# Performance work log

Hardware: AMD Instinct MI355X
Metric: run time of the kernel (lower is better)

## Reference

```python
import jax, jax.numpy as jnp
import numpy as np

EPS = 1e-5

def _bn(x, w, b, rm, rv):
    # eval-mode BatchNorm over channel axis (x: [..., C] broadcastable)
    return (x - rm) * (w * jax.lax.rsqrt(rv + EPS)) + b

def setup_inputs() -> dict:
    key = jax.random.key(0)
    ks = jax.random.split(key, 20)
    B, C, H, W = 2, 64, 96, 96
    Cq = C // 8  # query/key channels
    Cr = C // 8  # SE reduction channels
    s = 0.05
    inp = {
        'x': jax.random.normal(ks[0], (B, C, H, W), jnp.float32),
        'wq': jax.random.normal(ks[1], (Cq, C), jnp.float32) * s,
        'bq': jnp.zeros((Cq,), jnp.float32),
        'wk': jax.random.normal(ks[2], (Cq, C), jnp.float32) * s,
        'bk': jnp.zeros((Cq,), jnp.float32),
        'wv': jax.random.normal(ks[3], (C, C), jnp.float32) * s,
        'bv': jnp.zeros((C,), jnp.float32),
        'gamma': jnp.full((1,), 0.5, jnp.float32),
        'bn_w': jnp.ones((C,), jnp.float32),
        'bn_b': jnp.zeros((C,), jnp.float32),
        'bn_rm': jax.random.normal(ks[4], (C,), jnp.float32) * 0.1,
        'bn_rv': jax.random.uniform(ks[5], (C,), jnp.float32) + 0.5,
        'se_w1': jax.random.normal(ks[6], (Cr, C), jnp.float32) * s,
        'se_b1': jnp.zeros((Cr,), jnp.float32),
        'se_bn1_w': jnp.ones((Cr,), jnp.float32),
        'se_bn1_b': jnp.zeros((Cr,), jnp.float32),
        'se_bn1_rm': jax.random.normal(ks[7], (Cr,), jnp.float32) * 0.1,
        'se_bn1_rv': jax.random.uniform(ks[8], (Cr,), jnp.float32) + 0.5,
        'se_w2': jax.random.normal(ks[9], (C, Cr), jnp.float32) * s,
        'se_b2': jnp.zeros((C,), jnp.float32),
        'se_bn2_w': jnp.ones((C,), jnp.float32),
        'se_bn2_b': jnp.zeros((C,), jnp.float32),
        'se_bn2_rm': jax.random.normal(ks[10], (C,), jnp.float32) * 0.1,
        'se_bn2_rv': jax.random.uniform(ks[11], (C,), jnp.float32) + 0.5,
    }
    return inp

def reference(x, wq, bq, wk, bk, wv, bv, gamma, bn_w, bn_b, bn_rm, bn_rv,
              se_w1, se_b1, se_bn1_w, se_bn1_b, se_bn1_rm, se_bn1_rv,
              se_w2, se_b2, se_bn2_w, se_bn2_b, se_bn2_rm, se_bn2_rv):
    B, C, H, W = x.shape
    N = H * W
    xf = x.reshape(B, C, N)
    # PAM branch: 1x1 conv projections
    q = jnp.einsum('oc,bcn->bno', wq, xf) + bq            # [B,N,C/8]
    k = jnp.einsum('oc,bcn->bon', wk, xf) + bk[:, None]    # [B,C/8,N]
    v = jnp.einsum('oc,bcn->bon', wv, xf) + bv[:, None]    # [B,C,N]
    energy = jnp.einsum('bno,bom->bnm', q, k)              # [B,N,N]
    attn = jax.nn.softmax(energy, axis=-1)
    # out[b,c,i] = sum_j v[b,c,j] * attn[b,i,j]  (bmm(V, attn^T))
    out = jnp.einsum('bcj,bij->bci', v, attn)
    out = gamma[0] * out
    out = _bn(out, bn_w[:, None], bn_b[:, None], bn_rm[:, None], bn_rv[:, None])
    pam = out.reshape(B, C, H, W)
    # SE branch: GAP + 1x1 conv-bn-relu x2, multiplicative gate
    a = xf.mean(axis=2)                                    # [B,C]
    a1 = jax.nn.relu(_bn(a @ se_w1.T + se_b1, se_bn1_w, se_bn1_b, se_bn1_rm, se_bn1_rv))
    a2 = jax.nn.relu(_bn(a1 @ se_w2.T + se_b2, se_bn2_w, se_bn2_b, se_bn2_rm, se_bn2_rv))
    se = x * a2[:, :, None, None]
    return x + se + pam
```

## Files before the change

### kernel.cpp

```cpp
#include <hip/hip_runtime.h>
#include <hip/hip_bf16.h>

#define B_SZ   2
#define C_CH   64
#define NQ     8
#define QKS    16
#define NPIX   9216
#define NKS    576
#define QBLKS  288
#define KPART  8
#define KEYS_P 1152
#define NCHUNK 18
#define SM_F   2080
#define NP4    2304
#define KSTEP2 1024
#define VSTEP  4096

typedef short bf16x8 __attribute__((ext_vector_type(8)));
typedef float f32x4  __attribute__((ext_vector_type(4)));
typedef float f32x16 __attribute__((ext_vector_type(16)));
typedef unsigned u32x4 __attribute__((ext_vector_type(4)));
typedef unsigned uint2v __attribute__((ext_vector_type(2)));

static __device__ __forceinline__ unsigned pack2bf(float a, float b){
    unsigned r;
    asm("v_cvt_pk_bf16_f32 %0, %1, %2" : "=v"(r) : "v"(a), "v"(b));
    return r;
}

__global__ __launch_bounds__(256) void prep_kernel(
    const float* __restrict__ x,
    const float* __restrict__ wq, const float* __restrict__ bq,
    const float* __restrict__ wk, const float* __restrict__ bk,
    const float* __restrict__ wv, const float* __restrict__ bv,
    __hip_bfloat16* __restrict__ qp, __hip_bfloat16* __restrict__ kp,
    __hip_bfloat16* __restrict__ vswz, float* __restrict__ amean)
{
    const int blk = blockIdx.x, tid = threadIdx.x;
    if (blk < 144){
        int t  = blk*256 + tid;
        int n  = (t % NP4) * 4;
        int c8 = (t / NP4) & 7;
        int b  = t / (NP4*8);
        c8 = __builtin_amdgcn_readfirstlane(c8);
        b  = __builtin_amdgcn_readfirstlane(b);
        float acc[8][4];
#pragma unroll
        for (int k = 0; k < 8; ++k){
            float bvv = bv[c8*8 + k];
            acc[k][0] = bvv; acc[k][1] = bvv; acc[k][2] = bvv; acc[k][3] = bvv;
        }
#pragma unroll 4
        for (int ci = 0; ci < C_CH; ++ci){
            const float4 xv = *reinterpret_cast<const float4*>(
                x + (size_t)(b*C_CH + ci)*NPIX + n);
#pragma unroll
            for (int k = 0; k < 8; ++k){
                float w = wv[(c8*8 + k)*C_CH + ci];
                acc[k][0] = fmaf(xv.x, w, acc[k][0]);
                acc[k][1] = fmaf(xv.y, w, acc[k][1]);
                acc[k][2] = fmaf(xv.z, w, acc[k][2]);
                acc[k][3] = fmaf(xv.w, w, acc[k][3]);
            }
        }
#pragma unroll
        for (int k = 0; k < 8; ++k){
            int c = c8*8 + k;
            size_t base = ((size_t)((b*NKS + (n >> 4))*2 + (c >> 5)))*512
                        + (((n >> 3) & 1) << 8) + ((c & 31) << 3) + (n & 7);
            unsigned long long wpk =
                (unsigned long long)pack2bf(acc[k][0], acc[k][1]) |
                ((unsigned long long)pack2bf(acc[k][2], acc[k][3]) << 32);
            *reinterpret_cast<unsigned long long*>(vswz + base) = wpk;
        }
    } else if (blk < 180){
        int t  = (blk - 144)*256 + tid;
        int n  = (t % NP4) * 4;
        int o8 = (t / NP4) & 1;
        int b  = t / (NP4*2);
        o8 = __builtin_amdgcn_readfirstlane(o8);
        b  = __builtin_amdgcn_readfirstlane(b);
        const bool isq = (o8 == 0);
        const float* w    = isq ? wq : wk;
        const float* bias = isq ? bq : bk;
        float acc[8][4];
#pragma unroll
        for (int k = 0; k < 8; ++k){
            float bb = bias[k];
            acc[k][0] = bb; acc[k][1] = bb; acc[k][2] = bb; acc[k][3] = bb;
        }
#pragma unroll 4
        for (int ci = 0; ci < C_CH; ++ci){
            const float4 xv = *reinterpret_cast<const float4*>(
                x + (size_t)(b*C_CH + ci)*NPIX + n);
#pragma unroll
            for (int k = 0; k < 8; ++k){
                float wv_ = w[k*C_CH + ci];
                acc[k][0] = fmaf(xv.x, wv_, acc[k][0]);
                acc[k][1] = fmaf(xv.y, wv_, acc[k][1]);
                acc[k][2] = fmaf(xv.z, wv_, acc[k][2]);
                acc[k][3] = fmaf(xv.w, wv_, acc[k][3]);
            }
        }
        if (isq){
#pragma unroll
            for (int k = 0; k < 8; ++k)
#pragma unroll
                for (int px = 0; px < 4; ++px) acc[k][px] *= 1.44269504f;
        }
        __hip_bfloat16* dst = isq ? qp : kp;
        u32x4 zr; zr[0] = 0; zr[1] = 0; zr[2] = 0; zr[3] = 0;
#pragma unroll
        for (int px = 0; px < 4; ++px){
            u32x4 row;
            row[0] = pack2bf(acc[0][px], acc[1][px]);
            row[1] = pack2bf(acc[2][px], acc[3][px]);
            row[2] = pack2bf(acc[4][px], acc[5][px]);
            row[3] = pack2bf(acc[6][px], acc[7][px]);
            __hip_bfloat16* d0 = dst + ((size_t)(b*NPIX + n + px))*QKS;
            *reinterpret_cast<u32x4*>(d0)     = row;
            *reinterpret_cast<u32x4*>(d0 + 8) = zr;
        }
    } else {
        int bc = blk - 180;
        float s = 0.f;
        for (int i = tid; i < NPIX; i += 256) s += x[(size_t)bc*NPIX + i];
#pragma unroll
        for (int o = 32; o > 0; o >>= 1) s += __shfl_down(s, o, 64);
        __shared__ float red[4];
        if ((tid & 63) == 0) red[tid >> 6] = s;
        __syncthreads();
        if (tid == 0) amean[bc] = (red[0] + red[1] + red[2] + red[3]) * (1.f / (float)NPIX);
    }
}

__global__ __launch_bounds__(512) void flash_fused(
    const __hip_bfloat16* __restrict__ qp,
    const __hip_bfloat16* __restrict__ kp,
    const __hip_bfloat16* __restrict__ vswz,
    const float* __restrict__ amean,
    const float* __restrict__ sw1, const float* __restrict__ sb1,
    const float* __restrict__ s1w, const float* __restrict__ s1b,
    const float* __restrict__ s1m, const float* __restrict__ s1v,
    const float* __restrict__ sw2, const float* __restrict__ sb2,
    const float* __restrict__ s2w, const float* __restrict__ s2b,
    const float* __restrict__ s2m, const float* __restrict__ s2v,
    const float* __restrict__ x,
    const float* __restrict__ gamma,
    const float* __restrict__ bnw, const float* __restrict__ bnb,
    const float* __restrict__ bnm, const float* __restrict__ bnv,
    float* __restrict__ out)
{
    __shared__ __align__(16) float sm[4*SM_F];

    const int qt2 = blockIdx.x, b = blockIdx.y;
    const int p  = threadIdx.x >> 6;
    const int l  = threadIdx.x & 63;
    const int lc = l & 31;
    const int lh = l >> 5;

    bf16x8 qfrag = *reinterpret_cast<const bf16x8*>(
        qp + ((size_t)(b*NPIX + qt2*32 + lc))*QKS + lh*8);

    bf16x8 ones;
#pragma unroll
    for (int i = 0; i < 8; ++i) ones[i] = (short)0x3F80;

    f32x16 zero16;
#pragma unroll
    for (int i = 0; i < 16; ++i) zero16[i] = 0.f;

    f32x16 Of0 = zero16, Of1 = zero16;
    f32x16 Lacc = zero16;

    const __hip_bfloat16* kptr = kp + ((size_t)(b*NPIX + p*KEYS_P + lc))*QKS + lh*8;
    const __hip_bfloat16* vptr = vswz + ((size_t)((b*NKS + p*(KEYS_P/16))*2))*512 + l*8;

    auto CHUNK = [&](const bf16x8& k0, const bf16x8& k1){
        bf16x8 vf[8];
#pragma unroll
        for (int t = 0; t < 8; ++t)
            vf[t] = *reinterpret_cast<const bf16x8*>(vptr + t*512);
        vptr += VSTEP;

        unsigned D[16];
#pragma unroll
        for (int kt = 0; kt < 2; ++kt){
            f32x16 s = __builtin_amdgcn_mfma_f32_32x32x16_bf16(
                kt ? k1 : k0, qfrag, zero16, 0, 0, 0);
#pragma unroll
            for (int g = 0; g < 4; ++g){
                float e0 = exp2f(s[4*g+0]), e1 = exp2f(s[4*g+1]);
                float e2 = exp2f(s[4*g+2]), e3 = exp2f(s[4*g+3]);
                D[kt*8 + g*2 + 0] = pack2bf(e0, e1);
                D[kt*8 + g*2 + 1] = pack2bf(e2, e3);
            }
        }
#pragma unroll
        for (int ks = 0; ks < 4; ++ks){
            const int base = (ks >> 1)*8 + (ks & 1)*4;
            uint2v r0 = __builtin_amdgcn_permlane32_swap(D[base+0], D[base+2], false, false);
            uint2v r1 = __builtin_amdgcn_permlane32_swap(D[base+1], D[base+3], false, false);
            u32x4 pu; pu[0] = r0[0]; pu[1] = r1[0]; pu[2] = r0[1]; pu[3] = r1[1];
            bf16x8 pf = __builtin_bit_cast(bf16x8, pu);
            Of0  = __builtin_amdgcn_mfma_f32_32x32x16_bf16(vf[ks*2+0], pf, Of0, 0, 0, 0);
            Of1  = __builtin_amdgcn_mfma_f32_32x32x16_bf16(vf[ks*2+1], pf, Of1, 0, 0, 0);
            Lacc = __builtin_amdgcn_mfma_f32_32x32x16_bf16(ones,       pf, Lacc, 0, 0, 0);
        }
    };

    bf16x8 kA0 = *reinterpret_cast<const bf16x8*>(kptr);
    bf16x8 kA1 = *reinterpret_cast<const bf16x8*>(kptr + 512);
    kptr += KSTEP2;
    bf16x8 kB0, kB1;
    for (int it = 0; it < (NCHUNK - 2)/2; ++it){
        kB0 = *reinterpret_cast<const bf16x8*>(kptr);
        kB1 = *reinterpret_cast<const bf16x8*>(kptr + 512);
        kptr += KSTEP2;
        CHUNK(kA0, kA1);
        kA0 = *reinterpret_cast<const bf16x8*>(kptr);
        kA1 = *reinterpret_cast<const bf16x8*>(kptr + 512);
        kptr += KSTEP2;
        CHUNK(kB0, kB1);
    }
    kB0 = *reinterpret_cast<const bf16x8*>(kptr);
    kB1 = *reinterpret_cast<const bf16x8*>(kptr + 512);
    CHUNK(kA0, kA1);
    CHUNK(kB0, kB1);

    float a1r;
    {
        int r8 = l & 7;
        float s = sb1[r8];
#pragma unroll 8
        for (int c = 0; c < C_CH; ++c)
            s = fmaf(amean[b*C_CH + c], sw1[r8*C_CH + c], s);
        s = (s - s1m[r8]) * (s1w[r8] * rsqrtf(s1v[r8] + 1e-5f)) + s1b[r8];
        a1r = fmaxf(s, 0.f);
    }

    if (p >= 4){
        const int ps = p - 4;
#pragma unroll
        for (int r = 0; r < 16; ++r){
            sm[ps*SM_F +        r*64 + l] = Of0[r];
            sm[ps*SM_F + 1024 + r*64 + l] = Of1[r];
        }
        if (l < 32) sm[ps*SM_F + 2048 + l] = Lacc[0];
    }
    __syncthreads();
    if (p < 4){
#pragma unroll
        for (int r = 0; r < 16; ++r){
            sm[p*SM_F +        r*64 + l] += Of0[r];
            sm[p*SM_F + 1024 + r*64 + l] += Of1[r];
        }
        if (l < 32) sm[p*SM_F + 2048 + l] += Lacc[0];
    }
    __syncthreads();

    {
        const int w8 = threadIdx.x >> 6;
        const int i  = lc;
        const int cg = w8*2 + lh;
        float gam = gamma[0];

        float a1g[8];
#pragma unroll
        for (int j = 0; j < 8; ++j) a1g[j] = __shfl(a1r, (l & 56) | j, 64);
        float a2v[4];
#pragma unroll
        for (int r = 0; r < 4; ++r){
            int c = cg*4 + r;
            float s = sb2[c];
#pragma unroll
            for (int j = 0; j < 8; ++j) s = fmaf(a1g[j], sw2[c*NQ + j], s);
            s = (s - s2m[c]) * (s2w[c] * rsqrtf(s2v[c] + 1e-5f)) + s2b[c];
            a2v[r] = fmaxf(s, 0.f);
        }

        float L = 0.f;
#pragma unroll
        for (int q = 0; q < 4; ++q) L += sm[q*SM_F + 2048 + i];
        float invL = 1.f / L;
        int n = qt2*32 + i;
#pragma unroll
        for (int r = 0; r < 4; ++r){
            int c = cg*4 + r;
            int c5   = c & 31;
            int reg  = (c5 & 3) + 4*(c5 >> 3);
            int lsrc = (c5 >> 2) & 1;
            int o    = (c >> 5)*1024 + reg*64 + lsrc*32 + i;
            float O = 0.f;
#pragma unroll
            for (int q = 0; q < 4; ++q) O += sm[q*SM_F + o];
            float pam = gam * O * invL;
            pam = (pam - bnm[c]) * (bnw[c] * rsqrtf(bnv[c] + 1e-5f)) + bnb[c];
            float xv = x[(size_t)(b*C_CH + c)*NPIX + n];
            out[(size_t)(b*C_CH + c)*NPIX + n] = fmaf(xv, a2v[r], xv + pam);
        }
    }
}

extern "C" void kernel_launch(void* const* d_in, const int* in_sizes, int n_in,
                              void* d_out, int out_size, void* d_ws, size_t ws_size,
                              hipStream_t stream)
{
    const float* x     = (const float*)d_in[0];
    const float* wq    = (const float*)d_in[1];
    const float* bq    = (const float*)d_in[2];
    const float* wk    = (const float*)d_in[3];
    const float* bk    = (const float*)d_in[4];
    const float* wv    = (const float*)d_in[5];
    const float* bv    = (const float*)d_in[6];
    const float* gamma = (const float*)d_in[7];
    const float* bnw   = (const float*)d_in[8];
    const float* bnb   = (const float*)d_in[9];
    const float* bnm   = (const float*)d_in[10];
    const float* bnv   = (const float*)d_in[11];
    const float* sw1   = (const float*)d_in[12];
    const float* sb1   = (const float*)d_in[13];
    const float* s1w   = (const float*)d_in[14];
    const float* s1b   = (const float*)d_in[15];
    const float* s1m   = (const float*)d_in[16];
    const float* s1v   = (const float*)d_in[17];
    const float* sw2   = (const float*)d_in[18];
    const float* sb2   = (const float*)d_in[19];
    const float* s2w   = (const float*)d_in[20];
    const float* s2b   = (const float*)d_in[21];
    const float* s2m   = (const float*)d_in[22];
    const float* s2v   = (const float*)d_in[23];

    size_t off = 0;
    auto give = [&](size_t bytes) -> void* {
        void* r = (char*)d_ws + off;
        off += (bytes + 255) & ~(size_t)255;
        return r;
    };
    __hip_bfloat16* qp   = (__hip_bfloat16*)give((size_t)B_SZ*NPIX*QKS*2);
    __hip_bfloat16* kp   = (__hip_bfloat16*)give((size_t)B_SZ*NPIX*QKS*2);
    __hip_bfloat16* vswz = (__hip_bfloat16*)give((size_t)B_SZ*C_CH*NPIX*2);
    float* amean = (float*)give((size_t)B_SZ*C_CH*4);

    prep_kernel<<<dim3(308), dim3(256), 0, stream>>>(x, wq, bq, wk, bk, wv, bv,
                                                     qp, kp, vswz, amean);
    flash_fused<<<dim3(QBLKS, B_SZ), dim3(512), 0, stream>>>(
        qp, kp, vswz, amean,
        sw1, sb1, s1w, s1b, s1m, s1v,
        sw2, sb2, s2w, s2b, s2m, s2v,
        x, gamma, bnw, bnb, bnm, bnv, (float*)d_out);
}
```

Measured before the change: 192.9 us.

## Halve key-split waves per block, use raw exp2, simplify shared-memory reduction

Each flash block now runs 4 waves instead of 8, with every wave covering twice as many keys. That removes one round of shared-memory accumulation and a barrier, and the launch bounds are changed to allow 4 blocks per CU. The SE gate computation is folded into the per-channel output loop, which now covers 8 channels per lane group. exp2f is replaced with the raw hardware exp2 builtin to avoid range-handling code. The trade-off is longer serial key loops per wave and less intra-block parallelism, relying on higher block occupancy to compensate.

```diff
diff --git a/kernel.cpp b/kernel.cpp
--- a/kernel.cpp
+++ b/kernel.cpp
@@ -8,9 +8,9 @@
 #define NPIX   9216
 #define NKS    576
 #define QBLKS  288
-#define KPART  8
-#define KEYS_P 1152
-#define NCHUNK 18
+#define KPART  4
+#define KEYS_P 2304
+#define NCHUNK 36
 #define SM_F   2080
 #define NP4    2304
 #define KSTEP2 1024
@@ -26,6 +26,10 @@
     unsigned r;
     asm("v_cvt_pk_bf16_f32 %0, %1, %2" : "=v"(r) : "v"(a), "v"(b));
     return r;
+}
+
+static __device__ __forceinline__ float exp2r(float x){
+    return __builtin_amdgcn_exp2f(x);
 }
 
 __global__ __launch_bounds__(256) void prep_kernel(
@@ -134,7 +138,7 @@
     }
 }
 
-__global__ __launch_bounds__(512) void flash_fused(
+__global__ __launch_bounds__(256, 4) void flash_fused(
     const __hip_bfloat16* __restrict__ qp,
     const __hip_bfloat16* __restrict__ kp,
     const __hip_bfloat16* __restrict__ vswz,
@@ -190,8 +194,8 @@
                 kt ? k1 : k0, qfrag, zero16, 0, 0, 0);
 #pragma unroll
             for (int g = 0; g < 4; ++g){
-                float e0 = exp2f(s[4*g+0]), e1 = exp2f(s[4*g+1]);
-                float e2 = exp2f(s[4*g+2]), e3 = exp2f(s[4*g+3]);
+                float e0 = exp2r(s[4*g+0]), e1 = exp2r(s[4*g+1]);
+                float e2 = exp2r(s[4*g+2]), e3 = exp2r(s[4*g+3]);
                 D[kt*8 + g*2 + 0] = pack2bf(e0, e1);
                 D[kt*8 + g*2 + 1] = pack2bf(e2, e3);
             }
@@ -239,45 +243,22 @@
         a1r = fmaxf(s, 0.f);
     }
 
-    if (p >= 4){
-        const int ps = p - 4;
-#pragma unroll
-        for (int r = 0; r < 16; ++r){
-            sm[ps*SM_F +        r*64 + l] = Of0[r];
-            sm[ps*SM_F + 1024 + r*64 + l] = Of1[r];
-        }
-        if (l < 32) sm[ps*SM_F + 2048 + l] = Lacc[0];
-    }
+#pragma unroll
+    for (int r = 0; r < 16; ++r){
+        sm[p*SM_F +        r*64 + l] = Of0[r];
+        sm[p*SM_F + 1024 + r*64 + l] = Of1[r];
+    }
+    if (l < 32) sm[p*SM_F + 2048 + l] = Lacc[0];
     __syncthreads();
-    if (p < 4){
-#pragma unroll
-        for (int r = 0; r < 16; ++r){
-            sm[p*SM_F +        r*64 + l] += Of0[r];
-            sm[p*SM_F + 1024 + r*64 + l] += Of1[r];
-        }
-        if (l < 32) sm[p*SM_F + 2048 + l] += Lacc[0];
-    }
-    __syncthreads();
 
     {
-        const int w8 = threadIdx.x >> 6;
-        const int i  = lc;
-        const int cg = w8*2 + lh;
+        const int i   = lc;
+        const int cgs = p*2 + lh;
         float gam = gamma[0];
 
         float a1g[8];
 #pragma unroll
         for (int j = 0; j < 8; ++j) a1g[j] = __shfl(a1r, (l & 56) | j, 64);
-        float a2v[4];
-#pragma unroll
-        for (int r = 0; r < 4; ++r){
-            int c = cg*4 + r;
-            float s = sb2[c];
-#pragma unroll
-            for (int j = 0; j < 8; ++j) s = fmaf(a1g[j], sw2[c*NQ + j], s);
-            s = (s - s2m[c]) * (s2w[c] * rsqrtf(s2v[c] + 1e-5f)) + s2b[c];
-            a2v[r] = fmaxf(s, 0.f);
-        }
 
         float L = 0.f;
 #pragma unroll
@@ -285,8 +266,14 @@
         float invL = 1.f / L;
         int n = qt2*32 + i;
 #pragma unroll
-        for (int r = 0; r < 4; ++r){
-            int c = cg*4 + r;
+        for (int r = 0; r < 8; ++r){
+            int c = cgs*8 + r;
+            float s = sb2[c];
+#pragma unroll
+            for (int j = 0; j < 8; ++j) s = fmaf(a1g[j], sw2[c*NQ + j], s);
+            s = (s - s2m[c]) * (s2w[c] * rsqrtf(s2v[c] + 1e-5f)) + s2b[c];
+            float a2v = fmaxf(s, 0.f);
+
             int c5   = c & 31;
             int reg  = (c5 & 3) + 4*(c5 >> 3);
             int lsrc = (c5 >> 2) & 1;
@@ -297,7 +284,7 @@
             float pam = gam * O * invL;
             pam = (pam - bnm[c]) * (bnw[c] * rsqrtf(bnv[c] + 1e-5f)) + bnb[c];
             float xv = x[(size_t)(b*C_CH + c)*NPIX + n];
-            out[(size_t)(b*C_CH + c)*NPIX + n] = fmaf(xv, a2v[r], xv + pam);
+            out[(size_t)(b*C_CH + c)*NPIX + n] = fmaf(xv, a2v, xv + pam);
         }
     }
 }
@@ -344,7 +331,7 @@
 
     prep_kernel<<<dim3(308), dim3(256), 0, stream>>>(x, wq, bq, wk, bk, wv, bv,
                                                      qp, kp, vswz, amean);
-    flash_fused<<<dim3(QBLKS, B_SZ), dim3(512), 0, stream>>>(
+    flash_fused<<<dim3(QBLKS, B_SZ), dim3(256), 0, stream>>>(
         qp, kp, vswz, amean,
         sw1, sb1, s1w, s1b, s1m, s1v,
         sw2, sb2, s2w, s2b, s2m, s2v,
```

After: 171.4 us. 1.13x faster.
